# Performance work log

Measured on AMD Instinct MI355X. Metric: run time of the kernel, lower is better.

The kernel has to match this reference:

```python
import jax, jax.numpy as jnp
import numpy as np

EMBED_DIM = 1024
NUM_HEADS = 16
HEAD_DIM = EMBED_DIM // NUM_HEADS
MLP_SIZE = 4096
LN_EPS = 1e-5


def setup_inputs() -> dict:
    key = jax.random.key(0)
    ks = jax.random.split(key, 12)
    d, f = EMBED_DIM, MLP_SIZE
    s = lambda fan_in: 1.0 / np.sqrt(fan_in)
    return {
        "x": jax.random.normal(ks[0], (2, 2048, d), dtype=jnp.float32),
        "ln1_g": jnp.ones((d,), jnp.float32),
        "ln1_b": jnp.zeros((d,), jnp.float32),
        "ln2_g": jnp.ones((d,), jnp.float32),
        "ln2_b": jnp.zeros((d,), jnp.float32),
        "w_qkv": jax.random.uniform(ks[1], (d, 3 * d), jnp.float32, -s(d), s(d)),
        "b_qkv": jax.random.uniform(ks[2], (3 * d,), jnp.float32, -s(d), s(d)),
        "w_proj": jax.random.uniform(ks[3], (d, d), jnp.float32, -s(d), s(d)),
        "b_proj": jax.random.uniform(ks[4], (d,), jnp.float32, -s(d), s(d)),
        "w_fc1": jax.random.uniform(ks[5], (d, f), jnp.float32, -s(d), s(d)),
        "b_fc1": jax.random.uniform(ks[6], (f,), jnp.float32, -s(d), s(d)),
        "w_fc2": jax.random.uniform(ks[7], (f, d), jnp.float32, -s(f), s(f)),
        "b_fc2": jax.random.uniform(ks[8], (d,), jnp.float32, -s(f), s(f)),
    }


def _layernorm(x, g, b):
    mu = jnp.mean(x, axis=-1, keepdims=True)
    var = jnp.mean(jnp.square(x - mu), axis=-1, keepdims=True)
    return (x - mu) * jax.lax.rsqrt(var + LN_EPS) * g + b


def reference(x, ln1_g, ln1_b, ln2_g, ln2_b, w_qkv, b_qkv, w_proj, b_proj,
              w_fc1, b_fc1, w_fc2, b_fc2):
    B, N, C = x.shape
    H, D = NUM_HEADS, HEAD_DIM
    scale = D ** -0.5

    # --- attention sub-block (pre-LN) ---
    h = _layernorm(x, ln1_g, ln1_b)
    qkv = h @ w_qkv + b_qkv                      # [B,N,3C]
    qkv = qkv.reshape(B, N, 3, H, D)
    q, k, v = (jnp.moveaxis(qkv, 2, 0)[i].transpose(0, 2, 1, 3) for i in range(3))  # each [B,H,N,D]
    attn = jnp.einsum("bhnd,bhmd->bhnm", q, k) * scale
    attn = jax.nn.softmax(attn, axis=-1)
    o = jnp.einsum("bhnm,bhmd->bhnd", attn, v)   # [B,H,N,D]
    o = o.transpose(0, 2, 1, 3).reshape(B, N, C)
    x = x + (o @ w_proj + b_proj)

    # --- MLP sub-block (pre-LN) ---
    h = _layernorm(x, ln2_g, ln2_b)
    h = jax.nn.gelu(h @ w_fc1 + b_fc1, approximate=False)
    x = x + (h @ w_fc2 + b_fc2)
    return x
```

## Files before the change

### kernel.cpp

```cpp
#include <hip/hip_runtime.h>
#include <hip/hip_bf16.h>

typedef __attribute__((ext_vector_type(8))) __bf16 bf16x8;
typedef __attribute__((ext_vector_type(4))) float f32x4;
typedef unsigned short u16;

__device__ __forceinline__ float bf2f(u16 u) {
    unsigned int i = ((unsigned int)u) << 16;
    return __builtin_bit_cast(float, i);
}
__device__ __forceinline__ u16 f2bf_u16(float f) {
    __hip_bfloat16 h = __float2bfloat16(f);
    return *(u16*)&h;
}
__device__ __forceinline__ float gelu_f(float v) {
    return 0.5f * v * (1.0f + erff(v * 0.70710678118654752440f));
}
__device__ __forceinline__ float fexp2(float x) {
#if __has_builtin(__builtin_amdgcn_exp2f)
    return __builtin_amdgcn_exp2f(x);
#else
    return __expf(x * 0.69314718055994530942f);
#endif
}
__device__ __forceinline__ float max3f(float a, float b, float c) {
    return fmaxf(fmaxf(a, b), c);
}
__device__ __forceinline__ bool is_f32(const unsigned* p) { return *p == 0x3F800000u; }
__device__ __forceinline__ void async16(const void* g, void* l) {
    __builtin_amdgcn_global_load_lds(
        (const __attribute__((address_space(1))) void*)g,
        (__attribute__((address_space(3))) void*)l, 16, 0, 0);
}

__device__ __forceinline__ void conv8(const void* src, u16* dst, long off, bool f32in) {
    if (f32in) {
        const float* s = (const float*)src + off;
        float4 a = *(const float4*)s, b = *(const float4*)(s + 4);
        u16 o[8] = {f2bf_u16(a.x), f2bf_u16(a.y), f2bf_u16(a.z), f2bf_u16(a.w),
                    f2bf_u16(b.x), f2bf_u16(b.y), f2bf_u16(b.z), f2bf_u16(b.w)};
        *(uint4*)(dst + off) = *(const uint4*)o;
    } else {
        *(uint4*)(dst + off) = *(const uint4*)((const u16*)src + off);
    }
}

__global__ __launch_bounds__(256) void conv_bias(
        const void* __restrict__ bq, const void* __restrict__ bp,
        const void* __restrict__ b1, const void* __restrict__ b2,
        u16* dbq, u16* dbp, u16* db1, u16* db2,
        const unsigned* __restrict__ dtp) {
    long e = ((long)blockIdx.x * 256 + threadIdx.x) * 8;
    if (e >= 9216L) return;
    bool f = is_f32(dtp);
    if      (e < 3072L) conv8(bq, dbq, e, f);
    else if (e < 4096L) conv8(bp, dbp, e - 3072L, f);
    else if (e < 8192L) conv8(b1, db1, e - 4096L, f);
    else                conv8(b2, db2, e - 8192L, f);
}

__global__ __launch_bounds__(256) void conv_t(const void* __restrict__ src,
                                              u16* __restrict__ dst,
                                              int K, int N,
                                              const unsigned* __restrict__ dtp) {
    const bool f32in = is_f32(dtp);
    __shared__ u16 T[64 * 68];
    int k0 = blockIdx.y * 64, n0 = blockIdx.x * 64;
    int t = threadIdx.x;
    int kr = t >> 2, nc = (t & 3) * 16;

    u16 tmp[16];
    if (f32in) {
        const float* s = (const float*)src + (size_t)(k0 + kr) * N + n0 + nc;
        float4 a = *(const float4*)s;
        float4 b = *(const float4*)(s + 4);
        float4 c = *(const float4*)(s + 8);
        float4 d = *(const float4*)(s + 12);
        tmp[0]=f2bf_u16(a.x);  tmp[1]=f2bf_u16(a.y);  tmp[2]=f2bf_u16(a.z);  tmp[3]=f2bf_u16(a.w);
        tmp[4]=f2bf_u16(b.x);  tmp[5]=f2bf_u16(b.y);  tmp[6]=f2bf_u16(b.z);  tmp[7]=f2bf_u16(b.w);
        tmp[8]=f2bf_u16(c.x);  tmp[9]=f2bf_u16(c.y);  tmp[10]=f2bf_u16(c.z); tmp[11]=f2bf_u16(c.w);
        tmp[12]=f2bf_u16(d.x); tmp[13]=f2bf_u16(d.y); tmp[14]=f2bf_u16(d.z); tmp[15]=f2bf_u16(d.w);
    } else {
        const u16* s = (const u16*)src + (size_t)(k0 + kr) * N + n0 + nc;
        *(uint4*)&tmp[0] = *(const uint4*)s;
        *(uint4*)&tmp[8] = *(const uint4*)(s + 8);
    }
    u16* dl = &T[kr * 68 + nc];
    #pragma unroll
    for (int j = 0; j < 4; ++j)
        *(uint2*)(dl + 4 * j) = *(const uint2*)&tmp[4 * j];
    __syncthreads();

    int nr = t >> 2, kc = (t & 3) * 16;
    u16 o[16];
    #pragma unroll
    for (int i = 0; i < 16; ++i) o[i] = T[(kc + i) * 68 + nr];
    u16* dp = dst + (size_t)(n0 + nr) * K + k0 + kc;
    *(uint4*)dp       = *(const uint4*)&o[0];
    *(uint4*)(dp + 8) = *(const uint4*)&o[8];
}

__global__ __launch_bounds__(256) void vt_prep(const u16* __restrict__ qkv,
                                               unsigned* __restrict__ vtg) {
    __shared__ unsigned Vt[64 * 32];
    int bx = blockIdx.x;
    int b = bx >> 9, h = (bx >> 5) & 15, kt = bx & 31;
    int t = threadIdx.x;
    int va = t & 31, vdc = t >> 5;
    size_t vb = ((size_t)(b * 2048 + kt * 64 + 2 * va)) * 3072 + 2048 + h * 64 + vdc * 8;
    uint4 v0 = *(const uint4*)(qkv + vb);
    uint4 v1 = *(const uint4*)(qkv + vb + 3072);
    const u16* p0 = (const u16*)&v0;
    const u16* p1 = (const u16*)&v1;
    #pragma unroll
    for (int j = 0; j < 8; ++j)
        Vt[(vdc * 8 + j) * 32 + va] = (unsigned)p0[j] | ((unsigned)p1[j] << 16);
    __syncthreads();
    int R = t >> 2, u = t & 3;
    unsigned* dst = vtg + (size_t)bx * 2048 + R * 32;
    const unsigned* src = &Vt[R * 32 + u * 8];
    *(uint4*)(dst + (((2 * u)     ^ (R & 7)) * 4)) = *(const uint4*)src;
    *(uint4*)(dst + (((2 * u + 1) ^ (R & 7)) * 4)) = *(const uint4*)(src + 4);
}

__global__ __launch_bounds__(256) void ln_first(const void* __restrict__ xin,
                                                const void* __restrict__ g,
                                                const void* __restrict__ b,
                                                __hip_bfloat16* __restrict__ out,
                                                const unsigned* __restrict__ dtp) {
    const bool f32in = is_f32(dtp);
    int row = blockIdx.x, t = threadIdx.x;
    size_t base = (size_t)row * 1024 + 4 * t;
    float v[4];
    if (f32in) {
        float4 f = *(const float4*)((const float*)xin + base);
        v[0] = f.x; v[1] = f.y; v[2] = f.z; v[3] = f.w;
    } else {
        ushort4 u = *(const ushort4*)((const __hip_bfloat16*)xin + base);
        v[0] = bf2f(u.x); v[1] = bf2f(u.y); v[2] = bf2f(u.z); v[3] = bf2f(u.w);
    }
    float s = v[0] + v[1] + v[2] + v[3];
    float s2 = v[0]*v[0] + v[1]*v[1] + v[2]*v[2] + v[3]*v[3];
    #pragma unroll
    for (int off = 32; off > 0; off >>= 1) {
        s  += __shfl_down(s, off);
        s2 += __shfl_down(s2, off);
    }
    __shared__ float red[8];
    int wave = t >> 6, lane = t & 63;
    if (lane == 0) { red[wave] = s; red[4 + wave] = s2; }
    __syncthreads();
    float S  = red[0] + red[1] + red[2] + red[3];
    float S2 = red[4] + red[5] + red[6] + red[7];
    float mean = S * (1.0f / 1024.0f);
    float var  = S2 * (1.0f / 1024.0f) - mean * mean;
    float rstd = rsqrtf(var + 1e-5f);
    float gg[4], bb[4];
    if (f32in) {
        float4 fg = *(const float4*)((const float*)g + 4 * t);
        float4 fb = *(const float4*)((const float*)b + 4 * t);
        gg[0]=fg.x; gg[1]=fg.y; gg[2]=fg.z; gg[3]=fg.w;
        bb[0]=fb.x; bb[1]=fb.y; bb[2]=fb.z; bb[3]=fb.w;
    } else {
        ushort4 ug = *(const ushort4*)((const __hip_bfloat16*)g + 4 * t);
        ushort4 ub = *(const ushort4*)((const __hip_bfloat16*)b + 4 * t);
        gg[0]=bf2f(ug.x); gg[1]=bf2f(ug.y); gg[2]=bf2f(ug.z); gg[3]=bf2f(ug.w);
        bb[0]=bf2f(ub.x); bb[1]=bf2f(ub.y); bb[2]=bf2f(ub.z); bb[3]=bf2f(ub.w);
    }
    #pragma unroll
    for (int i = 0; i < 4; ++i)
        out[base + i] = __float2bfloat16((v[i] - mean) * rstd * gg[i] + bb[i]);
}

__global__ __launch_bounds__(256) void ln_mid(const float* __restrict__ x,
                                              const void* __restrict__ g,
                                              const void* __restrict__ b,
                                              __hip_bfloat16* __restrict__ out,
                                              const unsigned* __restrict__ dtp) {
    const bool f32in = is_f32(dtp);
    int row = blockIdx.x, t = threadIdx.x;
    size_t base = (size_t)row * 1024 + 4 * t;
    float4 f = *(const float4*)(x + base);
    float v[4] = {f.x, f.y, f.z, f.w};
    float s = v[0] + v[1] + v[2] + v[3];
    float s2 = v[0]*v[0] + v[1]*v[1] + v[2]*v[2] + v[3]*v[3];
    #pragma unroll
    for (int off = 32; off > 0; off >>= 1) {
        s  += __shfl_down(s, off);
        s2 += __shfl_down(s2, off);
    }
    __shared__ float red[8];
    int wave = t >> 6, lane = t & 63;
    if (lane == 0) { red[wave] = s; red[4 + wave] = s2; }
    __syncthreads();
    float S  = red[0] + red[1] + red[2] + red[3];
    float S2 = red[4] + red[5] + red[6] + red[7];
    float mean = S * (1.0f / 1024.0f);
    float var  = S2 * (1.0f / 1024.0f) - mean * mean;
    float rstd = rsqrtf(var + 1e-5f);
    float gg[4], bb[4];
    if (f32in) {
        float4 fg = *(const float4*)((const float*)g + 4 * t);
        float4 fb = *(const float4*)((const float*)b + 4 * t);
        gg[0]=fg.x; gg[1]=fg.y; gg[2]=fg.z; gg[3]=fg.w;
        bb[0]=fb.x; bb[1]=fb.y; bb[2]=fb.z; bb[3]=fb.w;
    } else {
        ushort4 ug = *(const ushort4*)((const __hip_bfloat16*)g + 4 * t);
        ushort4 ub = *(const ushort4*)((const __hip_bfloat16*)b + 4 * t);
        gg[0]=bf2f(ug.x); gg[1]=bf2f(ug.y); gg[2]=bf2f(ug.z); gg[3]=bf2f(ug.w);
        bb[0]=bf2f(ub.x); bb[1]=bf2f(ub.y); bb[2]=bf2f(ub.z); bb[3]=bf2f(ub.w);
    }
    #pragma unroll
    for (int i = 0; i < 4; ++i)
        out[base + i] = __float2bfloat16((v[i] - mean) * rstd * gg[i] + bb[i]);
}

template<int EPI, int BM, int BN, int BK>
__global__ __launch_bounds__(256, 2)
void gemm_bf16(const u16* __restrict__ A,
               const u16* __restrict__ BT,
               const u16* __restrict__ bias,
               const void* __restrict__ res,
               void* __restrict__ outp,
               int M, int N, int K,
               const unsigned* __restrict__ dtp) {
    constexpr int NI = BM / 32, NJ = BN / 32;
    constexpr int ASZ = BM * BK, BSZ = BN * BK;
    constexpr int SMASK = BK / 8 - 1;
    constexpr int SBITS = (BK == 32) ? 2 : 3;
    constexpr int RPA   = 512 / BK;
    constexpr int NASYA = (BM * BK) / 2048;
    constexpr int NASYB = (BN * BK) / 2048;
    const bool f32in = is_f32(dtp);
    __shared__ __align__(16) u16 As[2 * ASZ];
    __shared__ __align__(16) u16 Bs[2 * BSZ];
    (void)M;

    int t = threadIdx.x;
    int w = t >> 6, lane = t & 63;
    int quad = lane >> 4, lq = lane & 15;
    int nwg  = gridDim.x * gridDim.y;
    int bid  = blockIdx.y * gridDim.x + blockIdx.x;
    int swz  = (bid & 7) * (nwg >> 3) + (bid >> 3);
    int bn = (swz % gridDim.x) * BN;
    int bm = (swz / gridDim.x) * BM;
    int wm = (w & 1) * (16 * NI), wn = (w >> 1) * (16 * NJ);

    int sr = lane >> SBITS;
    int scs = ((lane & SMASK) ^ (sr & SMASK)) * 8;
    u16* aldst = &As[w * (BM * BK / 4) + lane * 8];
    const u16* ag = A + (size_t)(bm + w * (BM / 4) + sr) * K + scs;
    u16* bldst = &Bs[w * (BN * BK / 4) + lane * 8];
    const u16* bg = BT + (size_t)(bn + w * (BN / 4) + sr) * K + scs;

    f32x4 acc[NI][NJ];
    #pragma unroll
    for (int i = 0; i < NI; ++i)
        #pragma unroll
        for (int j = 0; j < NJ; ++j)
            #pragma unroll
            for (int r = 0; r < 4; ++r) acc[i][j][r] = 0.0f;

    #pragma unroll
    for (int j = 0; j < NASYA; ++j)
        async16(ag + (size_t)(j * RPA) * K, aldst + j * 512);
    #pragma unroll
    for (int j = 0; j < NASYB; ++j)
        async16(bg + (size_t)(j * RPA) * K, bldst + j * 512);

    const int nIter = K / BK;
    for (int k = 0; k < nIter; ++k) {
        __syncthreads();
        int cur = k & 1;
        if (k + 1 < nIter) {
            int nxt = cur ^ 1;
            const u16* agn = ag + (size_t)(k + 1) * BK;
            #pragma unroll
            for (int j = 0; j < NASYA; ++j)
                async16(agn + (size_t)(j * RPA) * K, aldst + nxt * ASZ + j * 512);
            const u16* bgn = bg + (size_t)(k + 1) * BK;
            #pragma unroll
            for (int j = 0; j < NASYB; ++j)
                async16(bgn + (size_t)(j * RPA) * K, bldst + nxt * BSZ + j * 512);
        }

        const u16* Ac = &As[cur * ASZ];
        const u16* Bc = &Bs[cur * BSZ];
        #pragma unroll
        for (int ks = 0; ks < BK / 32; ++ks) {
            bf16x8 af[NI], bfr[NJ];
            #pragma unroll
            for (int i = 0; i < NI; ++i) {
                int R = wm + 16 * i + lq;
                af[i] = *(const bf16x8*)&Ac[R * BK + ((quad + ks * 4) ^ (R & SMASK)) * 8];
            }
            #pragma unroll
            for (int j = 0; j < NJ; ++j) {
                int R = wn + 16 * j + lq;
                bfr[j] = *(const bf16x8*)&Bc[R * BK + ((quad + ks * 4) ^ (R & SMASK)) * 8];
            }
            #pragma unroll
            for (int i = 0; i < NI; ++i)
                #pragma unroll
                for (int j = 0; j < NJ; ++j)
                    acc[i][j] = __builtin_amdgcn_mfma_f32_16x16x32_bf16(af[i], bfr[j], acc[i][j], 0, 0, 0);
        }
    }

    #pragma unroll
    for (int i = 0; i < NI; ++i) {
        #pragma unroll
        for (int j = 0; j < NJ; ++j) {
            #pragma unroll
            for (int r = 0; r < 4; ++r) {
                int row = bm + wm + 16 * i + quad * 4 + r;
                int col = bn + wn + 16 * j + lq;
                size_t idx = (size_t)row * N + col;
                float v = acc[i][j][r] + bf2f(bias[col]);
                if constexpr (EPI == 0) {
                    ((__hip_bfloat16*)outp)[idx] = __float2bfloat16(v);
                } else if constexpr (EPI == 1) {
                    v += f32in ? ((const float*)res)[idx]
                               : bf2f(((const u16*)res)[idx]);
                    ((float*)outp)[idx] = v;
                } else if constexpr (EPI == 2) {
                    ((__hip_bfloat16*)outp)[idx] = __float2bfloat16(gelu_f(v));
                } else {
                    v += ((const float*)res)[idx];
                    if (f32in) ((float*)outp)[idx] = v;
                    else       ((__hip_bfloat16*)outp)[idx] = __float2bfloat16(v);
                }
            }
        }
    }
}

__global__ __launch_bounds__(256, 4)
void attn_mfma(const __hip_bfloat16* __restrict__ qkv,
               const unsigned* __restrict__ vtg,
               __hip_bfloat16* __restrict__ o_out) {
    __shared__ __align__(16) u16      Ks[2][64 * 64];
    __shared__ __align__(16) unsigned Vt[2][64 * 32];
    __shared__ __align__(16) u16      Ps[64 * 64];

    int t = threadIdx.x;
    int lane = t & 63, w = t >> 6;
    int quad = lane >> 4, lq = lane & 15;
    int bxh = blockIdx.x;
    int bx  = (bxh & 7) * 128 + (bxh >> 3);
    int b  = bx >> 9, h = (bx >> 5) & 15, qt = bx & 31;
    size_t tok0 = (size_t)b * 2048;

    int srow  = w * 16 + (lane >> 3);
    int kslot = ((lane & 7) ^ (lane >> 3)) * 8;
    const u16* kg = (const u16*)qkv + (tok0 + srow) * 3072 + 1024 + h * 64 + kslot;
    const unsigned* vg = vtg + ((size_t)(b * 512 + h * 32)) * 2048 + w * 512 + lane * 4;
    u16*      kd = &Ks[0][0] + w * 1024 + lane * 8;
    unsigned* vd = &Vt[0][0] + w * 512  + lane * 4;

    async16(kg, kd);
    async16(kg + (size_t)8 * 3072, kd + 512);
    async16(vg, vd);
    async16(vg + 256, vd + 256);

    {
        int key = t >> 2, ld = (t & 3) * 16;
        size_t qb = (tok0 + (size_t)qt * 64 + key) * 3072 + h * 64 + ld;
        uint4 a0 = *(const uint4*)(qkv + qb);
        uint4 a1 = *(const uint4*)(qkv + qb + 8);
        const u16* s0 = (const u16*)&a0;
        const u16* s1 = (const u16*)&a1;
        u16 q16[16];
        #pragma unroll
        for (int j = 0; j < 8; ++j) {
            q16[j]     = f2bf_u16(bf2f(s0[j]) * 0.125f);
            q16[8 + j] = f2bf_u16(bf2f(s1[j]) * 0.125f);
        }
        int k7 = key & 7;
        #pragma unroll
        for (int j4 = 0; j4 < 4; ++j4) {
            int c = ld + 4 * j4;
            *(uint2*)&Ps[key * 64 + (((c >> 3) ^ k7) * 8) + (c & 7)] =
                *(const uint2*)&q16[4 * j4];
        }
    }
    __syncthreads();

    int x7 = lq & 7;
    int Rq = w * 16 + lq;
    bf16x8 qf0 = *(const bf16x8*)&Ps[Rq * 64 + ((quad ^ x7) * 8)];
    bf16x8 qf1 = *(const bf16x8*)&Ps[Rq * 64 + (((4 + quad) ^ x7) * 8)];

    f32x4 oacc[4];
    #pragma unroll
    for (int dt = 0; dt < 4; ++dt)
        #pragma unroll
        for (int r = 0; r < 4; ++r) oacc[dt][r] = 0.0f;
    const float L2E = 1.44269504f;
    float m_run = -1e30f, l_run = 0.0f;
    float m2 = m_run * L2E;

    for (int kt = 0; kt < 32; ++kt) {
        int cur = kt & 1;
        if (kt) __syncthreads();
        if (kt + 1 < 32) {
            int nxt = cur ^ 1;
            const u16* kn = kg + (size_t)(kt + 1) * 64 * 3072;
            async16(kn, kd + nxt * 4096);
            async16(kn + (size_t)8 * 3072, kd + nxt * 4096 + 512);
            const unsigned* vn = vg + (size_t)(kt + 1) * 2048;
            async16(vn, vd + nxt * 2048);
            async16(vn + 256, vd + nxt * 2048 + 256);
        }

        const u16* KC = &Ks[0][0] + cur * 4096;
        f32x4 sacc[4];
        #pragma unroll
        for (int j = 0; j < 4; ++j)
            #pragma unroll
            for (int r = 0; r < 4; ++r) sacc[j][r] = 0.0f;
        __builtin_amdgcn_s_setprio(1);
        #pragma unroll
        for (int j = 0; j < 4; ++j) {
            int R = j * 16 + lq;
            bf16x8 kf0 = *(const bf16x8*)&KC[R * 64 + ((quad ^ x7) * 8)];
            bf16x8 kf1 = *(const bf16x8*)&KC[R * 64 + (((4 + quad) ^ x7) * 8)];
            sacc[j] = __builtin_amdgcn_mfma_f32_16x16x32_bf16(kf0, qf0, sacc[j], 0, 0, 0);
            sacc[j] = __builtin_amdgcn_mfma_f32_16x16x32_bf16(kf1, qf1, sacc[j], 0, 0, 0);
        }
        __builtin_amdgcn_s_setprio(0);

        float a0 = max3f(sacc[0][0], sacc[0][1], sacc[0][2]);
        float a1 = max3f(sacc[0][3], sacc[1][0], sacc[1][1]);
        float a2 = max3f(sacc[1][2], sacc[1][3], sacc[2][0]);
        float a3 = max3f(sacc[2][1], sacc[2][2], sacc[2][3]);
        float a4 = max3f(sacc[3][0], sacc[3][1], sacc[3][2]);
        float mx = fmaxf(max3f(a0, a1, a2), max3f(a3, a4, sacc[3][3]));
        mx = fmaxf(mx, __shfl_xor(mx, 16));
        mx = fmaxf(mx, __shfl_xor(mx, 32));
        if (!__all(mx <= m_run + 8.0f)) {
            float mnew = fmaxf(m_run, mx);
            float alpha = __expf(m_run - mnew);
            l_run *= alpha;
            #pragma unroll
            for (int dt = 0; dt < 4; ++dt)
                #pragma unroll
                for (int r = 0; r < 4; ++r) oacc[dt][r] *= alpha;
            m_run = mnew;
            m2 = m_run * L2E;
        }

        float ls = 0.0f;
        int prow = Rq * 64;
        #pragma unroll
        for (int j = 0; j < 4; ++j) {
            float p0 = fexp2(__builtin_fmaf(sacc[j][0], L2E, -m2));
            float p1 = fexp2(__builtin_fmaf(sacc[j][1], L2E, -m2));
            float p2 = fexp2(__builtin_fmaf(sacc[j][2], L2E, -m2));
            float p3 = fexp2(__builtin_fmaf(sacc[j][3], L2E, -m2));
            ls += (p0 + p1) + (p2 + p3);
            u16 pk[4] = {f2bf_u16(p0), f2bf_u16(p1), f2bf_u16(p2), f2bf_u16(p3)};
            int c = quad * 4 + 16 * j;
            *(uint2*)&Ps[prow + (((c >> 3) ^ x7) * 8) + (c & 7)] = *(const uint2*)pk;
        }
        ls += __shfl_xor(ls, 16);
        ls += __shfl_xor(ls, 32);
        l_run += ls;

        bf16x8 pf0 = *(const bf16x8*)&Ps[prow + ((quad ^ x7) * 8)];
        bf16x8 pf1 = *(const bf16x8*)&Ps[prow + (((4 + quad) ^ x7) * 8)];
        const unsigned* VC = &Vt[0][0] + cur * 2048;
        __builtin_amdgcn_s_setprio(1);
        #pragma unroll
        for (int dt = 0; dt < 4; ++dt) {
            int R = dt * 16 + lq;
            bf16x8 vf0 = __builtin_bit_cast(bf16x8, *(const uint4*)&VC[R * 32 + ((quad ^ x7) * 4)]);
            bf16x8 vf1 = __builtin_bit_cast(bf16x8, *(const uint4*)&VC[R * 32 + (((4 + quad) ^ x7) * 4)]);
            oacc[dt] = __builtin_amdgcn_mfma_f32_16x16x32_bf16(vf0, pf0, oacc[dt], 0, 0, 0);
            oacc[dt] = __builtin_amdgcn_mfma_f32_16x16x32_bf16(vf1, pf1, oacc[dt], 0, 0, 0);
        }
        __builtin_amdgcn_s_setprio(0);
    }

    __syncthreads();
    u16* T = &Ks[0][0];
    float inv = 1.0f / l_run;
    int trow = (w * 16 + lq) * 68;
    #pragma unroll
    for (int dt = 0; dt < 4; ++dt) {
        u16 pk[4] = {f2bf_u16(oacc[dt][0] * inv), f2bf_u16(oacc[dt][1] * inv),
                     f2bf_u16(oacc[dt][2] * inv), f2bf_u16(oacc[dt][3] * inv)};
        *(uint2*)&T[trow + quad * 4 + 16 * dt] = *(const uint2*)pk;
    }
    __syncthreads();
    {
        int q = t >> 2, dc = (t & 3) * 16;
        const u16* src = &T[q * 68 + dc];
        uint2 a0 = *(const uint2*)src;
        uint2 a1 = *(const uint2*)(src + 4);
        uint2 a2 = *(const uint2*)(src + 8);
        uint2 a3 = *(const uint2*)(src + 12);
        u16* op = (u16*)o_out + (tok0 + (size_t)qt * 64 + q) * 1024 + h * 64 + dc;
        *(uint4*)op       = make_uint4(a0.x, a0.y, a1.x, a1.y);
        *(uint4*)(op + 8) = make_uint4(a2.x, a2.y, a3.x, a3.y);
    }
}

extern "C" void kernel_launch(void* const* d_in, const int* in_sizes, int n_in,
                              void* d_out, int out_size, void* d_ws, size_t ws_size,
                              hipStream_t stream) {
    (void)in_sizes; (void)n_in; (void)out_size; (void)ws_size;
    const void* x      = d_in[0];
    const void* ln1_g  = d_in[1];
    const void* ln1_b  = d_in[2];
    const void* ln2_g  = d_in[3];
    const void* ln2_b  = d_in[4];
    const void* w_qkv  = d_in[5];
    const void* b_qkv  = d_in[6];
    const void* w_proj = d_in[7];
    const void* b_proj = d_in[8];
    const void* w_fc1  = d_in[9];
    const void* b_fc1  = d_in[10];
    const void* w_fc2  = d_in[11];
    const void* b_fc2  = d_in[12];
    const unsigned* probe = (const unsigned*)ln1_g;

    constexpr int Mtok = 4096;
    char* ws = (char*)d_ws;
    __hip_bfloat16* bufA = (__hip_bfloat16*)ws;
    __hip_bfloat16* qkvb = (__hip_bfloat16*)(ws + ((size_t)8 << 20));
    float*          x1   = (float*)(ws + ((size_t)8 << 20));
    u16*            w1T  = (u16*)(ws + ((size_t)24 << 20));
    u16*            wqT  = (u16*)(ws + ((size_t)32 << 20));
    u16*            wpT  = (u16*)(ws + ((size_t)38 << 20));
    unsigned*       vtg  = (unsigned*)(ws + ((size_t)40 << 20));
    __hip_bfloat16* g1   = (__hip_bfloat16*)(ws + ((size_t)32 << 20));
    u16*            w2T  = (u16*)ws;
    char* BZ = ws + ((size_t)64 << 20);
    u16* bqb = (u16*)BZ;
    u16* bpb = (u16*)(BZ + 8192);
    u16* b1b = (u16*)(BZ + 16384);
    u16* b2b = (u16*)(BZ + 24576);

    conv_bias<<<5, 256, 0, stream>>>(b_qkv, b_proj, b_fc1, b_fc2,
                                     bqb, bpb, b1b, b2b, probe);
    conv_t<<<dim3(3072 / 64, 1024 / 64), 256, 0, stream>>>(w_qkv, wqT, 1024, 3072, probe);
    conv_t<<<dim3(1024 / 64, 1024 / 64), 256, 0, stream>>>(w_proj, wpT, 1024, 1024, probe);
    ln_first<<<Mtok, 256, 0, stream>>>(x, ln1_g, ln1_b, bufA, probe);
    gemm_bf16<0, 128, 128, 32><<<dim3(3072 / 128, Mtok / 128), 256, 0, stream>>>(
        (const u16*)bufA, wqT, bqb, nullptr, qkvb, Mtok, 3072, 1024, probe);
    vt_prep<<<1024, 256, 0, stream>>>((const u16*)qkvb, vtg);
    attn_mfma<<<1024, 256, 0, stream>>>(qkvb, vtg, bufA);
    conv_t<<<dim3(4096 / 64, 1024 / 64), 256, 0, stream>>>(w_fc1, w1T, 1024, 4096, probe);
    gemm_bf16<1, 64, 64, 64><<<dim3(1024 / 64, Mtok / 64), 256, 0, stream>>>(
        (const u16*)bufA, wpT, bpb, x, x1, Mtok, 1024, 1024, probe);
    ln_mid<<<Mtok, 256, 0, stream>>>(x1, ln2_g, ln2_b, bufA, probe);
    gemm_bf16<2, 128, 128, 32><<<dim3(4096 / 128, Mtok / 128), 256, 0, stream>>>(
        (const u16*)bufA, w1T, b1b, nullptr, g1, Mtok, 4096, 1024, probe);
    conv_t<<<dim3(1024 / 64, 4096 / 64), 256, 0, stream>>>(w_fc2, w2T, 4096, 1024, probe);
    gemm_bf16<3, 64, 64, 64><<<dim3(1024 / 64, Mtok / 64), 256, 0, stream>>>(
        (const u16*)g1, w2T, b2b, x1, d_out, Mtok, 1024, 4096, probe);
}
```

Before: 365.7 us.

## Process two query tiles per attention block to reuse K/V tiles

Each attention workgroup now handles two 64-row query tiles that share every K/V tile loaded into LDS, which halves the grid and the K/V global traffic per query. The online-softmax state, accumulators and P buffers are duplicated, raising register pressure, and launch bounds are relaxed from 4 to 2 waves per SIMD. The cost is lower occupancy and fewer workgroups (512) to fill the GPU, while the MFMA work interleaved per loaded tile increases.

```diff
diff --git a/kernel.cpp b/kernel.cpp
--- a/kernel.cpp
+++ b/kernel.cpp
@@ -335,20 +335,21 @@
     }
 }
 
-__global__ __launch_bounds__(256, 4)
+__global__ __launch_bounds__(256, 2)
 void attn_mfma(const __hip_bfloat16* __restrict__ qkv,
                const unsigned* __restrict__ vtg,
                __hip_bfloat16* __restrict__ o_out) {
     __shared__ __align__(16) u16      Ks[2][64 * 64];
     __shared__ __align__(16) unsigned Vt[2][64 * 32];
-    __shared__ __align__(16) u16      Ps[64 * 64];
+    __shared__ __align__(16) u16      Ps[2][64 * 64];
 
     int t = threadIdx.x;
     int lane = t & 63, w = t >> 6;
     int quad = lane >> 4, lq = lane & 15;
     int bxh = blockIdx.x;
-    int bx  = (bxh & 7) * 128 + (bxh >> 3);
-    int b  = bx >> 9, h = (bx >> 5) & 15, qt = bx & 31;
+    int bx  = (bxh & 7) * 64 + (bxh >> 3);
+    int b  = bx >> 8, h = (bx >> 4) & 15, qt2 = bx & 15;
+    int qtA = qt2 * 2, qtB = qtA + 1;
     size_t tok0 = (size_t)b * 2048;
 
     int srow  = w * 16 + (lane >> 3);
@@ -365,40 +366,45 @@
 
     {
         int key = t >> 2, ld = (t & 3) * 16;
-        size_t qb = (tok0 + (size_t)qt * 64 + key) * 3072 + h * 64 + ld;
-        uint4 a0 = *(const uint4*)(qkv + qb);
-        uint4 a1 = *(const uint4*)(qkv + qb + 8);
-        const u16* s0 = (const u16*)&a0;
-        const u16* s1 = (const u16*)&a1;
-        u16 q16[16];
-        #pragma unroll
-        for (int j = 0; j < 8; ++j) {
-            q16[j]     = f2bf_u16(bf2f(s0[j]) * 0.125f);
-            q16[8 + j] = f2bf_u16(bf2f(s1[j]) * 0.125f);
-        }
         int k7 = key & 7;
         #pragma unroll
-        for (int j4 = 0; j4 < 4; ++j4) {
-            int c = ld + 4 * j4;
-            *(uint2*)&Ps[key * 64 + (((c >> 3) ^ k7) * 8) + (c & 7)] =
-                *(const uint2*)&q16[4 * j4];
+        for (int p = 0; p < 2; ++p) {
+            size_t qb = (tok0 + (size_t)(qtA + p) * 64 + key) * 3072 + h * 64 + ld;
+            uint4 a0 = *(const uint4*)(qkv + qb);
+            uint4 a1 = *(const uint4*)(qkv + qb + 8);
+            const u16* s0 = (const u16*)&a0;
+            const u16* s1 = (const u16*)&a1;
+            u16 q16[16];
+            #pragma unroll
+            for (int j = 0; j < 8; ++j) {
+                q16[j]     = f2bf_u16(bf2f(s0[j]) * 0.125f);
+                q16[8 + j] = f2bf_u16(bf2f(s1[j]) * 0.125f);
+            }
+            #pragma unroll
+            for (int j4 = 0; j4 < 4; ++j4) {
+                int c = ld + 4 * j4;
+                *(uint2*)&Ps[p][key * 64 + (((c >> 3) ^ k7) * 8) + (c & 7)] =
+                    *(const uint2*)&q16[4 * j4];
+            }
         }
     }
     __syncthreads();
 
     int x7 = lq & 7;
     int Rq = w * 16 + lq;
-    bf16x8 qf0 = *(const bf16x8*)&Ps[Rq * 64 + ((quad ^ x7) * 8)];
-    bf16x8 qf1 = *(const bf16x8*)&Ps[Rq * 64 + (((4 + quad) ^ x7) * 8)];
-
-    f32x4 oacc[4];
+    bf16x8 qfA0 = *(const bf16x8*)&Ps[0][Rq * 64 + ((quad ^ x7) * 8)];
+    bf16x8 qfA1 = *(const bf16x8*)&Ps[0][Rq * 64 + (((4 + quad) ^ x7) * 8)];
+    bf16x8 qfB0 = *(const bf16x8*)&Ps[1][Rq * 64 + ((quad ^ x7) * 8)];
+    bf16x8 qfB1 = *(const bf16x8*)&Ps[1][Rq * 64 + (((4 + quad) ^ x7) * 8)];
+
+    f32x4 oaccA[4], oaccB[4];
     #pragma unroll
     for (int dt = 0; dt < 4; ++dt)
         #pragma unroll
-        for (int r = 0; r < 4; ++r) oacc[dt][r] = 0.0f;
+        for (int r = 0; r < 4; ++r) { oaccA[dt][r] = 0.0f; oaccB[dt][r] = 0.0f; }
     const float L2E = 1.44269504f;
-    float m_run = -1e30f, l_run = 0.0f;
-    float m2 = m_run * L2E;
+    float m_runA = -1e30f, l_runA = 0.0f, m2A = m_runA * L2E;
+    float m_runB = -1e30f, l_runB = 0.0f, m2B = m_runB * L2E;
 
     for (int kt = 0; kt < 32; ++kt) {
         int cur = kt & 1;
@@ -414,61 +420,102 @@
         }
 
         const u16* KC = &Ks[0][0] + cur * 4096;
-        f32x4 sacc[4];
+        f32x4 sA[4], sB[4];
         #pragma unroll
         for (int j = 0; j < 4; ++j)
             #pragma unroll
-            for (int r = 0; r < 4; ++r) sacc[j][r] = 0.0f;
+            for (int r = 0; r < 4; ++r) { sA[j][r] = 0.0f; sB[j][r] = 0.0f; }
         __builtin_amdgcn_s_setprio(1);
         #pragma unroll
         for (int j = 0; j < 4; ++j) {
             int R = j * 16 + lq;
             bf16x8 kf0 = *(const bf16x8*)&KC[R * 64 + ((quad ^ x7) * 8)];
             bf16x8 kf1 = *(const bf16x8*)&KC[R * 64 + (((4 + quad) ^ x7) * 8)];
-            sacc[j] = __builtin_amdgcn_mfma_f32_16x16x32_bf16(kf0, qf0, sacc[j], 0, 0, 0);
-            sacc[j] = __builtin_amdgcn_mfma_f32_16x16x32_bf16(kf1, qf1, sacc[j], 0, 0, 0);
+            sA[j] = __builtin_amdgcn_mfma_f32_16x16x32_bf16(kf0, qfA0, sA[j], 0, 0, 0);
+            sA[j] = __builtin_amdgcn_mfma_f32_16x16x32_bf16(kf1, qfA1, sA[j], 0, 0, 0);
+            sB[j] = __builtin_amdgcn_mfma_f32_16x16x32_bf16(kf0, qfB0, sB[j], 0, 0, 0);
+            sB[j] = __builtin_amdgcn_mfma_f32_16x16x32_bf16(kf1, qfB1, sB[j], 0, 0, 0);
         }
         __builtin_amdgcn_s_setprio(0);
 
-        float a0 = max3f(sacc[0][0], sacc[0][1], sacc[0][2]);
-        float a1 = max3f(sacc[0][3], sacc[1][0], sacc[1][1]);
-        float a2 = max3f(sacc[1][2], sacc[1][3], sacc[2][0]);
-        float a3 = max3f(sacc[2][1], sacc[2][2], sacc[2][3]);
-        float a4 = max3f(sacc[3][0], sacc[3][1], sacc[3][2]);
-        float mx = fmaxf(max3f(a0, a1, a2), max3f(a3, a4, sacc[3][3]));
-        mx = fmaxf(mx, __shfl_xor(mx, 16));
-        mx = fmaxf(mx, __shfl_xor(mx, 32));
-        if (!__all(mx <= m_run + 8.0f)) {
-            float mnew = fmaxf(m_run, mx);
-            float alpha = __expf(m_run - mnew);
-            l_run *= alpha;
-            #pragma unroll
-            for (int dt = 0; dt < 4; ++dt)
+        int prow = Rq * 64;
+        {
+            float a0 = max3f(sA[0][0], sA[0][1], sA[0][2]);
+            float a1 = max3f(sA[0][3], sA[1][0], sA[1][1]);
+            float a2 = max3f(sA[1][2], sA[1][3], sA[2][0]);
+            float a3 = max3f(sA[2][1], sA[2][2], sA[2][3]);
+            float a4 = max3f(sA[3][0], sA[3][1], sA[3][2]);
+            float mx = fmaxf(max3f(a0, a1, a2), max3f(a3, a4, sA[3][3]));
+            mx = fmaxf(mx, __shfl_xor(mx, 16));
+            mx = fmaxf(mx, __shfl_xor(mx, 32));
+            if (!__all(mx <= m_runA + 8.0f)) {
+                float mnew = fmaxf(m_runA, mx);
+                float alpha = __expf(m_runA - mnew);
+                l_runA *= alpha;
                 #pragma unroll
-                for (int r = 0; r < 4; ++r) oacc[dt][r] *= alpha;
-            m_run = mnew;
-            m2 = m_run * L2E;
-        }
-
-        float ls = 0.0f;
-        int prow = Rq * 64;
-        #pragma unroll
-        for (int j = 0; j < 4; ++j) {
-            float p0 = fexp2(__builtin_fmaf(sacc[j][0], L2E, -m2));
-            float p1 = fexp2(__builtin_fmaf(sacc[j][1], L2E, -m2));
-            float p2 = fexp2(__builtin_fmaf(sacc[j][2], L2E, -m2));
-            float p3 = fexp2(__builtin_fmaf(sacc[j][3], L2E, -m2));
-            ls += (p0 + p1) + (p2 + p3);
-            u16 pk[4] = {f2bf_u16(p0), f2bf_u16(p1), f2bf_u16(p2), f2bf_u16(p3)};
-            int c = quad * 4 + 16 * j;
-            *(uint2*)&Ps[prow + (((c >> 3) ^ x7) * 8) + (c & 7)] = *(const uint2*)pk;
-        }
-        ls += __shfl_xor(ls, 16);
-        ls += __shfl_xor(ls, 32);
-        l_run += ls;
-
-        bf16x8 pf0 = *(const bf16x8*)&Ps[prow + ((quad ^ x7) * 8)];
-        bf16x8 pf1 = *(const bf16x8*)&Ps[prow + (((4 + quad) ^ x7) * 8)];
+                for (int dt = 0; dt < 4; ++dt)
+                    #pragma unroll
+                    for (int r = 0; r < 4; ++r) oaccA[dt][r] *= alpha;
+                m_runA = mnew;
+                m2A = m_runA * L2E;
+            }
+            float ls = 0.0f;
+            #pragma unroll
+            for (int j = 0; j < 4; ++j) {
+                float p0 = fexp2(__builtin_fmaf(sA[j][0], L2E, -m2A));
+                float p1 = fexp2(__builtin_fmaf(sA[j][1], L2E, -m2A));
+                float p2 = fexp2(__builtin_fmaf(sA[j][2], L2E, -m2A));
+                float p3 = fexp2(__builtin_fmaf(sA[j][3], L2E, -m2A));
+                ls += (p0 + p1) + (p2 + p3);
+                u16 pk[4] = {f2bf_u16(p0), f2bf_u16(p1), f2bf_u16(p2), f2bf_u16(p3)};
+                int c = quad * 4 + 16 * j;
+                *(uint2*)&Ps[0][prow + (((c >> 3) ^ x7) * 8) + (c & 7)] = *(const uint2*)pk;
+            }
+            ls += __shfl_xor(ls, 16);
+            ls += __shfl_xor(ls, 32);
+            l_runA += ls;
+        }
+        {
+            float a0 = max3f(sB[0][0], sB[0][1], sB[0][2]);
+            float a1 = max3f(sB[0][3], sB[1][0], sB[1][1]);
+            float a2 = max3f(sB[1][2], sB[1][3], sB[2][0]);
+            float a3 = max3f(sB[2][1], sB[2][2], sB[2][3]);
+            float a4 = max3f(sB[3][0], sB[3][1], sB[3][2]);
+            float mx = fmaxf(max3f(a0, a1, a2), max3f(a3, a4, sB[3][3]));
+            mx = fmaxf(mx, __shfl_xor(mx, 16));
+            mx = fmaxf(mx, __shfl_xor(mx, 32));
+            if (!__all(mx <= m_runB + 8.0f)) {
+                float mnew = fmaxf(m_runB, mx);
+                float alpha = __expf(m_runB - mnew);
+                l_runB *= alpha;
+                #pragma unroll
+                for (int dt = 0; dt < 4; ++dt)
+                    #pragma unroll
+                    for (int r = 0; r < 4; ++r) oaccB[dt][r] *= alpha;
+                m_runB = mnew;
+                m2B = m_runB * L2E;
+            }
+            float ls = 0.0f;
+            #pragma unroll
+            for (int j = 0; j < 4; ++j) {
+                float p0 = fexp2(__builtin_fmaf(sB[j][0], L2E, -m2B));
+                float p1 = fexp2(__builtin_fmaf(sB[j][1], L2E, -m2B));
+                float p2 = fexp2(__builtin_fmaf(sB[j][2], L2E, -m2B));
+                float p3 = fexp2(__builtin_fmaf(sB[j][3], L2E, -m2B));
+                ls += (p0 + p1) + (p2 + p3);
+                u16 pk[4] = {f2bf_u16(p0), f2bf_u16(p1), f2bf_u16(p2), f2bf_u16(p3)};
+                int c = quad * 4 + 16 * j;
+                *(uint2*)&Ps[1][prow + (((c >> 3) ^ x7) * 8) + (c & 7)] = *(const uint2*)pk;
+            }
+            ls += __shfl_xor(ls, 16);
+            ls += __shfl_xor(ls, 32);
+            l_runB += ls;
+        }
+
+        bf16x8 pA0 = *(const bf16x8*)&Ps[0][prow + ((quad ^ x7) * 8)];
+        bf16x8 pA1 = *(const bf16x8*)&Ps[0][prow + (((4 + quad) ^ x7) * 8)];
+        bf16x8 pB0 = *(const bf16x8*)&Ps[1][prow + ((quad ^ x7) * 8)];
+        bf16x8 pB1 = *(const bf16x8*)&Ps[1][prow + (((4 + quad) ^ x7) * 8)];
         const unsigned* VC = &Vt[0][0] + cur * 2048;
         __builtin_amdgcn_s_setprio(1);
         #pragma unroll
@@ -476,31 +523,53 @@
             int R = dt * 16 + lq;
             bf16x8 vf0 = __builtin_bit_cast(bf16x8, *(const uint4*)&VC[R * 32 + ((quad ^ x7) * 4)]);
             bf16x8 vf1 = __builtin_bit_cast(bf16x8, *(const uint4*)&VC[R * 32 + (((4 + quad) ^ x7) * 4)]);
-            oacc[dt] = __builtin_amdgcn_mfma_f32_16x16x32_bf16(vf0, pf0, oacc[dt], 0, 0, 0);
-            oacc[dt] = __builtin_amdgcn_mfma_f32_16x16x32_bf16(vf1, pf1, oacc[dt], 0, 0, 0);
+            oaccA[dt] = __builtin_amdgcn_mfma_f32_16x16x32_bf16(vf0, pA0, oaccA[dt], 0, 0, 0);
+            oaccA[dt] = __builtin_amdgcn_mfma_f32_16x16x32_bf16(vf1, pA1, oaccA[dt], 0, 0, 0);
+            oaccB[dt] = __builtin_amdgcn_mfma_f32_16x16x32_bf16(vf0, pB0, oaccB[dt], 0, 0, 0);
+            oaccB[dt] = __builtin_amdgcn_mfma_f32_16x16x32_bf16(vf1, pB1, oaccB[dt], 0, 0, 0);
         }
         __builtin_amdgcn_s_setprio(0);
     }
 
     __syncthreads();
     u16* T = &Ks[0][0];
-    float inv = 1.0f / l_run;
-    int trow = (w * 16 + lq) * 68;
-    #pragma unroll
-    for (int dt = 0; dt < 4; ++dt) {
-        u16 pk[4] = {f2bf_u16(oacc[dt][0] * inv), f2bf_u16(oacc[dt][1] * inv),
-                     f2bf_u16(oacc[dt][2] * inv), f2bf_u16(oacc[dt][3] * inv)};
-        *(uint2*)&T[trow + quad * 4 + 16 * dt] = *(const uint2*)pk;
-    }
-    __syncthreads();
+    int trow = Rq * 68;
     {
+        float inv = 1.0f / l_runA;
+        #pragma unroll
+        for (int dt = 0; dt < 4; ++dt) {
+            u16 pk[4] = {f2bf_u16(oaccA[dt][0] * inv), f2bf_u16(oaccA[dt][1] * inv),
+                         f2bf_u16(oaccA[dt][2] * inv), f2bf_u16(oaccA[dt][3] * inv)};
+            *(uint2*)&T[trow + quad * 4 + 16 * dt] = *(const uint2*)pk;
+        }
+        __syncthreads();
         int q = t >> 2, dc = (t & 3) * 16;
         const u16* src = &T[q * 68 + dc];
         uint2 a0 = *(const uint2*)src;
         uint2 a1 = *(const uint2*)(src + 4);
         uint2 a2 = *(const uint2*)(src + 8);
         uint2 a3 = *(const uint2*)(src + 12);
-        u16* op = (u16*)o_out + (tok0 + (size_t)qt * 64 + q) * 1024 + h * 64 + dc;
+        u16* op = (u16*)o_out + (tok0 + (size_t)qtA * 64 + q) * 1024 + h * 64 + dc;
+        *(uint4*)op       = make_uint4(a0.x, a0.y, a1.x, a1.y);
+        *(uint4*)(op + 8) = make_uint4(a2.x, a2.y, a3.x, a3.y);
+    }
+    __syncthreads();
+    {
+        float inv = 1.0f / l_runB;
+        #pragma unroll
+        for (int dt = 0; dt < 4; ++dt) {
+            u16 pk[4] = {f2bf_u16(oaccB[dt][0] * inv), f2bf_u16(oaccB[dt][1] * inv),
+                         f2bf_u16(oaccB[dt][2] * inv), f2bf_u16(oaccB[dt][3] * inv)};
+            *(uint2*)&T[trow + quad * 4 + 16 * dt] = *(const uint2*)pk;
+        }
+        __syncthreads();
+        int q = t >> 2, dc = (t & 3) * 16;
+        const u16* src = &T[q * 68 + dc];
+        uint2 a0 = *(const uint2*)src;
+        uint2 a1 = *(const uint2*)(src + 4);
+        uint2 a2 = *(const uint2*)(src + 8);
+        uint2 a3 = *(const uint2*)(src + 12);
+        u16* op = (u16*)o_out + (tok0 + (size_t)qtB * 64 + q) * 1024 + h * 64 + dc;
         *(uint4*)op       = make_uint4(a0.x, a0.y, a1.x, a1.y);
         *(uint4*)(op + 8) = make_uint4(a2.x, a2.y, a3.x, a3.y);
     }
@@ -550,7 +619,7 @@
     gemm_bf16<0, 128, 128, 32><<<dim3(3072 / 128, Mtok / 128), 256, 0, stream>>>(
         (const u16*)bufA, wqT, bqb, nullptr, qkvb, Mtok, 3072, 1024, probe);
     vt_prep<<<1024, 256, 0, stream>>>((const u16*)qkvb, vtg);
-    attn_mfma<<<1024, 256, 0, stream>>>(qkvb, vtg, bufA);
+    attn_mfma<<<512, 256, 0, stream>>>(qkvb, vtg, bufA);
     conv_t<<<dim3(4096 / 64, 1024 / 64), 256, 0, stream>>>(w_fc1, w1T, 1024, 4096, probe);
     gemm_bf16<1, 64, 64, 64><<<dim3(1024 / 64, Mtok / 64), 256, 0, stream>>>(
         (const u16*)bufA, wpT, bpb, x, x1, Mtok, 1024, 1024, probe);
```

After: 357.3 us (median of 2 runs). 1.02x faster.
